# Performance work log

Hardware: AMD Instinct MI355X
Metric: run time of the kernel (lower is better)

## Reference

```python
import jax, jax.numpy as jnp
import numpy as np

LN_EPS = 1e-5

def _layernorm(x, g, b):
    mu = jnp.mean(x, axis=-1, keepdims=True)
    var = jnp.mean(jnp.square(x - mu), axis=-1, keepdims=True)
    return (x - mu) * jax.lax.rsqrt(var + LN_EPS) * g + b

def setup_inputs() -> dict:
    key = jax.random.key(0)
    ks = jax.random.split(key, 12)
    B, S, E = 8, 4096, 512
    H, DK = 64, 8          # d_k = E // H = 8 qubits per head
    NQ_FFN, FFN = 8, 2048
    TWO_PI = 2.0 * np.pi
    x = jax.random.normal(ks[0], (B, S, E), dtype=jnp.float32)
    # trainable RX phases per attention head/wire; trainable RY phases for FFN qubits
    theta_attn = jax.random.uniform(ks[1], (H, DK), dtype=jnp.float32, maxval=TWO_PI)
    theta_ffn = jax.random.uniform(ks[2], (NQ_FFN,), dtype=jnp.float32, maxval=TWO_PI)
    s_e = 1.0 / np.sqrt(E)
    W_comb = jax.random.uniform(ks[3], (E, E), dtype=jnp.float32, minval=-s_e, maxval=s_e)
    b_comb = jax.random.uniform(ks[4], (E,), dtype=jnp.float32, minval=-s_e, maxval=s_e)
    s_q = 1.0 / np.sqrt(NQ_FFN)
    W1 = jax.random.uniform(ks[5], (FFN, NQ_FFN), dtype=jnp.float32, minval=-s_q, maxval=s_q)
    b1 = jax.random.uniform(ks[6], (FFN,), dtype=jnp.float32, minval=-s_q, maxval=s_q)
    s_f = 1.0 / np.sqrt(FFN)
    W2 = jax.random.uniform(ks[7], (E, FFN), dtype=jnp.float32, minval=-s_f, maxval=s_f)
    b2 = jax.random.uniform(ks[8], (E,), dtype=jnp.float32, minval=-s_f, maxval=s_f)
    ln1_g = jnp.ones((E,), jnp.float32); ln1_b = jnp.zeros((E,), jnp.float32)
    ln2_g = jnp.ones((E,), jnp.float32); ln2_b = jnp.zeros((E,), jnp.float32)
    return {"x": x, "theta_attn": theta_attn, "W_comb": W_comb, "b_comb": b_comb,
            "ln1_g": ln1_g, "ln1_b": ln1_b, "theta_ffn": theta_ffn,
            "W1": W1, "b1": b1, "W2": W2, "b2": b2, "ln2_g": ln2_g, "ln2_b": ln2_b}

def reference(x, theta_attn, W_comb, b_comb, ln1_g, ln1_b, theta_ffn, W1, b1, W2, b2, ln2_g, ln2_b):
    B, S, E = x.shape
    H, DK = theta_attn.shape
    NQ = theta_ffn.shape[0]
    # Quantum attention heads: RX(x) then RX(theta) on |0> per wire -> <Z> = cos(x+theta)
    q = jnp.cos(x.reshape(B, S, H, DK) + theta_attn)  # [B,S,H,DK]
    attn_out = jnp.einsum('bse,fe->bsf', q.reshape(B, S, E), W_comb) + b_comb
    x1 = _layernorm(x + attn_out, ln1_g, ln1_b)
    # Quantum FFN layer: RY(x) then RY(theta) -> <Z> = cos(x+theta), first NQ features only
    fq = jnp.cos(x1[..., :NQ] + theta_ffn)            # [B,S,NQ]
    h = jax.nn.relu(jnp.einsum('bsq,fq->bsf', fq, W1) + b1)
    ffn_out = jnp.einsum('bsf,ef->bse', h, W2) + b2
    return _layernorm(x1 + ffn_out, ln2_g, ln2_b)
```

## Files before the change

kernel.cpp:

```cpp
#include <hip/hip_runtime.h>
#include <stdint.h>

typedef unsigned short u16;
typedef __bf16 bf16x8 __attribute__((ext_vector_type(8)));
typedef float f32x4 __attribute__((ext_vector_type(4)));

#define AS1(p) ((const __attribute__((address_space(1))) void*)(p))
#define AS3(p) ((__attribute__((address_space(3))) void*)(p))

__device__ __forceinline__ float b2f(u16 v){
    union { unsigned u; float f; } x; x.u = ((unsigned)v) << 16; return x.f;
}
__device__ __forceinline__ u16 f2b(float f){
    union { float f; unsigned u; } x; x.f = f;
    unsigned r = x.u + 0x7FFFu + ((x.u >> 16) & 1u);
    return (u16)(r >> 16);
}

__global__ __launch_bounds__(256) void probe_kernel(
    const u16* p0,const u16* p1,const u16* p2,const u16* p3,const u16* p4,
    const u16* p5,const u16* p6,const u16* p7,const u16* p8,const u16* p9,
    const u16* p10,const u16* p11,const u16* p12,
    int n0,int n1,int n2,int n3,int n4,int n5,int n6,int n7,int n8,int n9,
    int n10,int n11,int n12, int* flags)
{
    const u16* p; int n;
    switch (blockIdx.x) {
        case 0: p=p0; n=n0; break;   case 1: p=p1; n=n1; break;
        case 2: p=p2; n=n2; break;   case 3: p=p3; n=n3; break;
        case 4: p=p4; n=n4; break;   case 5: p=p5; n=n5; break;
        case 6: p=p6; n=n6; break;   case 7: p=p7; n=n7; break;
        case 8: p=p8; n=n8; break;   case 9: p=p9; n=n9; break;
        case 10: p=p10; n=n10; break; case 11: p=p11; n=n11; break;
        default: p=p12; n=n12; break;
    }
    int pairs = n >> 1; if (pairs > 2048) pairs = 2048;
    int strong = 0, znz = 0, tot = 0;
    for (int k = threadIdx.x; k < pairs; k += 256) {
        u16 lo = p[2*k], hi = p[2*k+1];
        int eh = (hi >> 7) & 0xFF;
        int el = (lo >> 7) & 0xFF;
        if (eh >= 0xF0 || (eh >= 1 && eh <= 0x40)) strong = 1;
        if (el >= 0xF0 || (el >= 1 && el <= 0x40)) strong = 1;
        if (lo == 0 && hi != 0) znz++;
        tot++;
    }
    __shared__ int ss, sz, st;
    if (threadIdx.x == 0) { ss = 0; sz = 0; st = 0; }
    __syncthreads();
    if (strong) atomicOr(&ss, 1);
    if (znz) atomicAdd(&sz, znz);
    atomicAdd(&st, tot);
    __syncthreads();
    if (threadIdx.x == 0) {
        flags[blockIdx.x] = (ss || (2 * sz > st)) ? 1 : 0;
        if (blockIdx.x == 0) flags[15] = 0;
    }
}

__global__ __launch_bounds__(256) void convert_kernel(
    const void* sWc, const void* sW2, const void* sW1,
    const void* sTa, const void* sBc, const void* sG1, const void* sB1l,
    const void* sTf, const void* sB1, const void* sB2, const void* sG2, const void* sB2l,
    u16* wbase, const int* flags)
{
    int b = blockIdx.x;
    const void* src; u16* dst; int n, fi, lb, tof32 = 0;
    if (b < 128)      { src=sWc; dst=wbase;          n=262144;  fi=2;  lb=b; }
    else if (b < 640) { src=sW2; dst=wbase+262144;   n=1048576; fi=9;  lb=b-128; }
    else if (b >= 643 && b < 651) { src=sW1; dst=wbase+1312256; n=16384; fi=7; lb=b-643; }
    else {
        lb = 0;
        switch (b) {
            case 640: src=sTa;  dst=wbase+1310720; n=512;  fi=1;  break;
            case 641: src=sBc;  dst=wbase+1311232; n=512;  fi=3;  break;
            case 642: src=sB2;  dst=wbase+1311744; n=512;  fi=10; break;
            case 651: src=sB1;  dst=wbase+1328640; n=2048; fi=8;  break;
            case 652: src=sG1;  dst=wbase+1330688; n=512;  fi=4;  break;
            case 653: src=sB1l; dst=wbase+1331200; n=512;  fi=5;  break;
            case 654: src=sG2;  dst=wbase+1331712; n=512;  fi=11; break;
            case 655: src=sB2l; dst=wbase+1332224; n=512;  fi=12; break;
            default:  src=sTf;  dst=wbase+1332736; n=8;    fi=6;  tof32=1; break;
        }
    }
    int i = lb * 256 + threadIdx.x;
    if (i * 8 >= n) return;
    if (tof32) {
        float* fd = (float*)dst;
        if (flags[fi]) {
            const float4* s = (const float4*)src;
            ((float4*)fd)[i*2] = s[i*2]; ((float4*)fd)[i*2+1] = s[i*2+1];
        } else {
            union { uint4 v; u16 h[8]; } sb;
            sb.v = ((const uint4*)src)[i];
            #pragma unroll
            for (int j = 0; j < 8; j++) fd[i*8+j] = b2f(sb.h[j]);
        }
        return;
    }
    if (flags[fi]) {
        const float4* s = (const float4*)src;
        float4 a = s[i*2], c = s[i*2+1];
        union { uint4 v; u16 h[8]; } o;
        o.h[0]=f2b(a.x); o.h[1]=f2b(a.y); o.h[2]=f2b(a.z); o.h[3]=f2b(a.w);
        o.h[4]=f2b(c.x); o.h[5]=f2b(c.y); o.h[6]=f2b(c.z); o.h[7]=f2b(c.w);
        ((uint4*)dst)[i] = o.v;
    } else {
        ((uint4*)dst)[i] = ((const uint4*)src)[i];
    }
}

__global__ __launch_bounds__(256) void gemm1_fused(
    const void* __restrict__ x, const u16* __restrict__ theta,
    const u16* __restrict__ Wt, const u16* __restrict__ bias,
    u16* __restrict__ dst, int mtiles, const int* flags)
{
    __shared__ __align__(16) u16 As[128 * 64];
    __shared__ __align__(16) u16 Bs[2][128 * 64];
    __shared__ __align__(16) u16 thlds[512];
    const int K = 512, N = 512;
    const int tid  = threadIdx.x;
    const int lane = tid & 63;
    const int w    = tid >> 6;

    const int blk = blockIdx.x;
    const int xcd = blk & 7;
    const int j   = blk >> 3;
    const int per = mtiles >> 3;
    const int mt  = xcd * per + (j >> 2);
    const int nt  = j & 3;
    const int m0 = mt * 128;
    const int n0 = nt * 128;

    const int srow = lane >> 3;
    const int scol = ((lane & 7) ^ srow) * 8;
    const int wm = (w >> 1) * 64;
    const int wn = (w & 1) * 64;
    const int fr   = lane & 15;
    const int quad = lane >> 4;
    const int fx   = fr & 7;

    const int genrow = tid & 127;
    const int khalf  = tid >> 7;
    const int isf32  = flags[0];

    if (tid < 64) ((uint4*)thlds)[tid] = ((const uint4*)theta)[tid];

    f32x4 acc[4][4];
    #pragma unroll
    for (int i = 0; i < 4; i++)
        #pragma unroll
        for (int jj = 0; jj < 4; jj++)
            acc[i][jj] = f32x4{0.f, 0.f, 0.f, 0.f};

    const u16* Bbase = Wt + (size_t)n0 * K + scol;

    #pragma unroll
    for (int i = 0; i < 4; i++) {
        int c = w * 4 + i;
        int row = c * 8 + srow;
        __builtin_amdgcn_global_load_lds(AS1(Bbase + (size_t)row * K),
                                         AS3(&Bs[0][c * 512]), 16, 0, 0);
    }
    uint4 xr[8];
    {
        size_t eoff = (size_t)(m0 + genrow) * 512 + khalf * 32;
        if (isf32) {
            const uint4* p = (const uint4*)x + (eoff >> 2);
            #pragma unroll
            for (int i = 0; i < 8; i++) xr[i] = p[i];
        } else {
            const uint4* p = (const uint4*)x + (eoff >> 3);
            #pragma unroll
            for (int i = 0; i < 4; i++) xr[i] = p[i];
        }
    }

    int cur = 0;
    for (int kt = 0; kt < K; kt += 64) {
        __syncthreads();
        {
            float xv[32];
            if (isf32) {
                const float* xf = (const float*)xr;
                #pragma unroll
                for (int i2 = 0; i2 < 32; i2++) xv[i2] = xf[i2];
            } else {
                const u16* xh = (const u16*)xr;
                #pragma unroll
                for (int i2 = 0; i2 < 32; i2++) xv[i2] = b2f(xh[i2]);
            }
            int tbase = (kt + khalf * 32) >> 3;
            #pragma unroll
            for (int jj = 0; jj < 4; jj++) {
                union { uint4 v; u16 h[8]; } tb;
                tb.v = ((const uint4*)thlds)[tbase + jj];
                union { uint4 v; __bf16 h[8]; } ob;
                #pragma unroll
                for (int e = 0; e < 8; e++)
                    ob.h[e] = (__bf16)__cosf(xv[jj * 8 + e] + b2f(tb.h[e]));
                int o = khalf * 4 + jj;
                *(uint4*)(As + genrow * 64 + ((o ^ (genrow & 7)) * 8)) = ob.v;
            }
        }
        __syncthreads();
        if (kt + 64 < K) {
            size_t eoff = (size_t)(m0 + genrow) * 512 + kt + 64 + khalf * 32;
            if (isf32) {
                const uint4* p = (const uint4*)x + (eoff >> 2);
                #pragma unroll
                for (int i = 0; i < 8; i++) xr[i] = p[i];
            } else {
                const uint4* p = (const uint4*)x + (eoff >> 3);
                #pragma unroll
                for (int i = 0; i < 4; i++) xr[i] = p[i];
            }
            int nxt = cur ^ 1;
            #pragma unroll
            for (int i = 0; i < 4; i++) {
                int c = w * 4 + i;
                int row = c * 8 + srow;
                __builtin_amdgcn_global_load_lds(
                    AS1(Bbase + (size_t)row * K + kt + 64),
                    AS3(&Bs[nxt][c * 512]), 16, 0, 0);
            }
        }
        #pragma unroll
        for (int kk = 0; kk < 2; kk++) {
            bf16x8 af[4], bfr[4];
            #pragma unroll
            for (int mi = 0; mi < 4; mi++)
                af[mi] = *(const bf16x8*)(As + (wm + mi * 16 + fr) * 64 +
                                          (((kk * 4 + quad) ^ fx) * 8));
            #pragma unroll
            for (int ni = 0; ni < 4; ni++)
                bfr[ni] = *(const bf16x8*)(&Bs[cur][(wn + ni * 16 + fr) * 64 +
                                           (((kk * 4 + quad) ^ fx) * 8)]);
            #pragma unroll
            for (int mi = 0; mi < 4; mi++)
                #pragma unroll
                for (int ni = 0; ni < 4; ni++)
                    acc[mi][ni] = __builtin_amdgcn_mfma_f32_16x16x32_bf16(
                        af[mi], bfr[ni], acc[mi][ni], 0, 0, 0);
        }
        cur ^= 1;
    }

    #pragma unroll
    for (int mi = 0; mi < 4; mi++) {
        #pragma unroll
        for (int ni = 0; ni < 4; ni++) {
            int n = n0 + wn + ni * 16 + fr;
            float bn = b2f(bias[n]);
            #pragma unroll
            for (int r = 0; r < 4; r++) {
                int m = m0 + wm + mi * 16 + quad * 4 + r;
                float rv = isf32 ? ((const float*)x)[(size_t)m * N + n]
                                 : b2f(((const u16*)x)[(size_t)m * N + n]);
                dst[(size_t)m * N + n] = f2b(acc[mi][ni][r] + bn + rv);
            }
        }
    }
}

__global__ __launch_bounds__(256) void gemm2_fused(
    const u16* __restrict__ fq, const u16* __restrict__ W1, const u16* __restrict__ b1,
    const u16* __restrict__ Wt, const u16* __restrict__ bias,
    const u16* __restrict__ res, u16* __restrict__ dst, int mtiles)
{
    __shared__ __align__(16) u16 As[128 * 64];
    __shared__ __align__(16) u16 Bs[2][128 * 64];
    const int K = 2048, N = 512;
    const int tid  = threadIdx.x;
    const int lane = tid & 63;
    const int w    = tid >> 6;

    const int blk = blockIdx.x;
    const int xcd = blk & 7;
    const int j   = blk >> 3;
    const int per = mtiles >> 3;
    const int mt  = xcd * per + (j >> 2);
    const int nt  = j & 3;
    const int m0 = mt * 128;
    const int n0 = nt * 128;

    const int srow = lane >> 3;
    const int scol = ((lane & 7) ^ srow) * 8;
    const int wm = (w >> 1) * 64;
    const int wn = (w & 1) * 64;
    const int fr   = lane & 15;
    const int quad = lane >> 4;
    const int fx   = fr & 7;

    bf16x8 fqf[8];
    #pragma unroll
    for (int t2 = 0; t2 < 8; t2++) {
        union { uint4 v; bf16x8 b; } z; z.v = uint4{0,0,0,0};
        if (quad == 0) z.v = *(const uint4*)(fq + (size_t)(m0 + t2 * 16 + fr) * 8);
        fqf[t2] = z.b;
    }
    union { uint4 v; bf16x8 b; } w1u; w1u.v = uint4{0,0,0,0};
    if (quad == 0) w1u.v = *(const uint4*)(W1 + (size_t)(w * 16 + fr) * 8);
    uint2 b1v = *(const uint2*)(b1 + w * 16 + quad * 4);

    f32x4 acc[4][4];
    #pragma unroll
    for (int i = 0; i < 4; i++)
        #pragma unroll
        for (int jj = 0; jj < 4; jj++)
            acc[i][jj] = f32x4{0.f, 0.f, 0.f, 0.f};

    const u16* Bbase = Wt + (size_t)n0 * K + scol;
    #pragma unroll
    for (int i = 0; i < 4; i++) {
        int c = w * 4 + i;
        int row = c * 8 + srow;
        __builtin_amdgcn_global_load_lds(AS1(Bbase + (size_t)row * K),
                                         AS3(&Bs[0][c * 512]), 16, 0, 0);
    }

    int cur = 0;
    for (int kt = 0; kt < K; kt += 64) {
        __syncthreads();
        {
            const u16* pb = (const u16*)&b1v;
            f32x4 binit = {b2f(pb[0]), b2f(pb[1]), b2f(pb[2]), b2f(pb[3])};
            const int g   = w * 2 + (quad >> 1);
            const int off = (quad & 1) * 4;
            #pragma unroll
            for (int t2 = 0; t2 < 8; t2++) {
                f32x4 hv = __builtin_amdgcn_mfma_f32_16x16x32_bf16(
                    w1u.b, fqf[t2], binit, 0, 0, 0);
                union { uint2 u; __bf16 h[4]; } hw;
                hw.h[0] = (__bf16)fmaxf(hv[0], 0.f);
                hw.h[1] = (__bf16)fmaxf(hv[1], 0.f);
                hw.h[2] = (__bf16)fmaxf(hv[2], 0.f);
                hw.h[3] = (__bf16)fmaxf(hv[3], 0.f);
                int m = t2 * 16 + fr;
                *(uint2*)(As + m * 64 + ((g ^ (m & 7)) * 8 + off)) = hw.u;
            }
        }
        __syncthreads();
        if (kt + 64 < K) {
            if (quad == 0)
                w1u.v = *(const uint4*)(W1 + (size_t)(kt + 64 + w * 16 + fr) * 8);
            b1v = *(const uint2*)(b1 + kt + 64 + w * 16 + quad * 4);
            int nxt = cur ^ 1;
            #pragma unroll
            for (int i = 0; i < 4; i++) {
                int c = w * 4 + i;
                int row = c * 8 + srow;
                __builtin_amdgcn_global_load_lds(
                    AS1(Bbase + (size_t)row * K + kt + 64),
                    AS3(&Bs[nxt][c * 512]), 16, 0, 0);
            }
        }
        #pragma unroll
        for (int kk = 0; kk < 2; kk++) {
            bf16x8 af[4], bfr[4];
            #pragma unroll
            for (int mi = 0; mi < 4; mi++)
                af[mi] = *(const bf16x8*)(As + (wm + mi * 16 + fr) * 64 +
                                          (((kk * 4 + quad) ^ fx) * 8));
            #pragma unroll
            for (int ni = 0; ni < 4; ni++)
                bfr[ni] = *(const bf16x8*)(&Bs[cur][(wn + ni * 16 + fr) * 64 +
                                           (((kk * 4 + quad) ^ fx) * 8)]);
            #pragma unroll
            for (int mi = 0; mi < 4; mi++)
                #pragma unroll
                for (int ni = 0; ni < 4; ni++)
                    acc[mi][ni] = __builtin_amdgcn_mfma_f32_16x16x32_bf16(
                        af[mi], bfr[ni], acc[mi][ni], 0, 0, 0);
        }
        cur ^= 1;
    }

    #pragma unroll
    for (int mi = 0; mi < 4; mi++) {
        #pragma unroll
        for (int ni = 0; ni < 4; ni++) {
            int n = n0 + wn + ni * 16 + fr;
            float bn = b2f(bias[n]);
            #pragma unroll
            for (int r = 0; r < 4; r++) {
                int m = m0 + wm + mi * 16 + quad * 4 + r;
                float rv = b2f(res[(size_t)m * N + n]);
                dst[(size_t)m * N + n] = f2b(acc[mi][ni][r] + bn + rv);
            }
        }
    }
}

__global__ __launch_bounds__(512) void ln1_kernel(
    const u16* __restrict__ y1, const u16* __restrict__ g, const u16* __restrict__ b,
    const float* __restrict__ tf, u16* __restrict__ x1, u16* __restrict__ fqout)
{
    __shared__ __align__(16) float xs8[64][8];
    const int t = threadIdx.x;
    const int wv = t >> 6, l = t & 63;
    const size_t rbase = (size_t)blockIdx.x * 64;

    union { uint4 v; u16 s[8]; } gb, bb;
    gb.v = *(const uint4*)(g + l * 8);
    bb.v = *(const uint4*)(b + l * 8);

    #pragma unroll
    for (int i = 0; i < 8; i++) {
        int lr = wv * 8 + i;
        union { uint4 v; u16 s[8]; } yb;
        yb.v = ((const uint4*)(y1 + (rbase + lr) * 512))[l];
        float xv[8], s = 0.f, ss = 0.f;
        #pragma unroll
        for (int jj = 0; jj < 8; jj++) {
            xv[jj] = b2f(yb.s[jj]); s += xv[jj]; ss += xv[jj] * xv[jj];
        }
        #pragma unroll
        for (int o = 32; o > 0; o >>= 1) { s += __shfl_down(s, o); ss += __shfl_down(ss, o); }
        s = __shfl(s, 0); ss = __shfl(ss, 0);
        float mu = s * (1.f / 512.f);
        float rs = rsqrtf(ss * (1.f / 512.f) - mu * mu + 1e-5f);
        union { uint4 v; u16 s[8]; } ob;
        float xn[8];
        #pragma unroll
        for (int jj = 0; jj < 8; jj++) {
            xn[jj] = (xv[jj] - mu) * rs * b2f(gb.s[jj]) + b2f(bb.s[jj]);
            ob.s[jj] = f2b(xn[jj]);
        }
        ((uint4*)(x1 + (rbase + lr) * 512))[l] = ob.v;
        if (l == 0) {
            #pragma unroll
            for (int jj = 0; jj < 8; jj++) xs8[lr][jj] = xn[jj];
        }
    }
    __syncthreads();
    {
        int r = t >> 3, jj = t & 7;
        fqout[(rbase + r) * 8 + jj] = f2b(__cosf(xs8[r][jj] + tf[jj]));
    }
}

__global__ __launch_bounds__(256) void ln2_kernel(
    const u16* __restrict__ z, const u16* __restrict__ g, const u16* __restrict__ b,
    void* __restrict__ out, const int* flags)
{
    const int t = threadIdx.x;
    const int wv = t >> 6, l = t & 63;
    const size_t row = (size_t)blockIdx.x * 4 + wv;

    union { uint4 v; u16 s[8]; } zb, gb, bb;
    zb.v = ((const uint4*)(z + row * 512))[l];
    gb.v = *(const uint4*)(g + l * 8);
    bb.v = *(const uint4*)(b + l * 8);
    float xv[8], s = 0.f, ss = 0.f;
    #pragma unroll
    for (int jj = 0; jj < 8; jj++) { xv[jj] = b2f(zb.s[jj]); s += xv[jj]; ss += xv[jj]*xv[jj]; }
    #pragma unroll
    for (int o = 32; o > 0; o >>= 1) { s += __shfl_down(s, o); ss += __shfl_down(ss, o); }
    s = __shfl(s, 0); ss = __shfl(ss, 0);
    float mu = s * (1.f / 512.f);
    float rs = rsqrtf(ss * (1.f / 512.f) - mu * mu + 1e-5f);
    float xn[8];
    #pragma unroll
    for (int jj = 0; jj < 8; jj++)
        xn[jj] = (xv[jj] - mu) * rs * b2f(gb.s[jj]) + b2f(bb.s[jj]);
    if (flags[0]) {
        float* po = (float*)out + row * 512 + l * 8;
        float4 o0{xn[0],xn[1],xn[2],xn[3]}, o1{xn[4],xn[5],xn[6],xn[7]};
        *(float4*)po = o0; *(float4*)(po + 4) = o1;
    } else {
        union { uint4 v; u16 s[8]; } ob;
        #pragma unroll
        for (int jj = 0; jj < 8; jj++) ob.s[jj] = f2b(xn[jj]);
        ((uint4*)((u16*)out + row * 512))[l] = ob.v;
    }
}

extern "C" void kernel_launch(void* const* d_in, const int* in_sizes, int n_in,
                              void* d_out, int out_size, void* d_ws, size_t ws_size,
                              hipStream_t stream)
{
    u16* ws16 = (u16*)d_ws;
    u16* W     = ws16;
    int* flags = (int*)(ws16 + 1332752);
    u16* fq  = ws16 + 1332800;
    u16* x1  = ws16 + 1594944;
    u16* y1  = ws16 + 18372160;
    u16* z   = y1;

    const u16*  wWc  = W;
    const u16*  wW2  = W + 262144;
    const u16*  wTa  = W + 1310720;
    const u16*  wBc  = W + 1311232;
    const u16*  wB2  = W + 1311744;
    const u16*  wW1  = W + 1312256;
    const u16*  wB1  = W + 1328640;
    const u16*  wG1  = W + 1330688;
    const u16*  wB1l = W + 1331200;
    const u16*  wG2  = W + 1331712;
    const u16*  wB2l = W + 1332224;
    const float* wTf = (const float*)(W + 1332736);

    probe_kernel<<<13, 256, 0, stream>>>(
        (const u16*)d_in[0], (const u16*)d_in[1], (const u16*)d_in[2],
        (const u16*)d_in[3], (const u16*)d_in[4], (const u16*)d_in[5],
        (const u16*)d_in[6], (const u16*)d_in[7], (const u16*)d_in[8],
        (const u16*)d_in[9], (const u16*)d_in[10], (const u16*)d_in[11],
        (const u16*)d_in[12],
        in_sizes[0], in_sizes[1], in_sizes[2], in_sizes[3], in_sizes[4],
        in_sizes[5], in_sizes[6], in_sizes[7], in_sizes[8], in_sizes[9],
        in_sizes[10], in_sizes[11], in_sizes[12], flags);

    convert_kernel<<<657, 256, 0, stream>>>(
        d_in[2], d_in[9], d_in[7], d_in[1], d_in[3], d_in[4], d_in[5],
        d_in[6], d_in[8], d_in[10], d_in[11], d_in[12], (u16*)W, flags);

    gemm1_fused<<<1024, 256, 0, stream>>>(
        d_in[0], wTa, wWc, wBc, y1, 256, flags);

    ln1_kernel<<<512, 512, 0, stream>>>(y1, wG1, wB1l, wTf, x1, fq);

    gemm2_fused<<<1024, 256, 0, stream>>>(
        fq, wW1, wB1, wW2, wB2, x1, z, 256);

    ln2_kernel<<<8192, 256, 0, stream>>>(z, wG2, wB2l, d_out, flags);
}
```

Baseline: 352.2 us.

## Compute cos(x+theta) A-fragments directly from global memory in gemm1

Removes the shared-memory staging tile for the A operand in the first GEMM. Each wave now loads x straight from global memory into its MFMA fragment registers and applies cos(x+theta) there. This drops one LDS buffer and one barrier per k-step and adds a launch-bounds occupancy hint. The cost is that x loads are no longer prefetched a step ahead, so load latency sits in the MFMA loop. The cosine is also recomputed by both waves that share the same rows (wn split), doubling the transcendental work and x reads.

```diff
diff --git a/kernel.cpp b/kernel.cpp
--- a/kernel.cpp
+++ b/kernel.cpp
@@ -110,12 +110,11 @@
     }
 }
 
-__global__ __launch_bounds__(256) void gemm1_fused(
+__global__ __launch_bounds__(256, 4) void gemm1_fused(
     const void* __restrict__ x, const u16* __restrict__ theta,
     const u16* __restrict__ Wt, const u16* __restrict__ bias,
     u16* __restrict__ dst, int mtiles, const int* flags)
 {
-    __shared__ __align__(16) u16 As[128 * 64];
     __shared__ __align__(16) u16 Bs[2][128 * 64];
     __shared__ __align__(16) u16 thlds[512];
     const int K = 512, N = 512;
@@ -139,10 +138,7 @@
     const int fr   = lane & 15;
     const int quad = lane >> 4;
     const int fx   = fr & 7;
-
-    const int genrow = tid & 127;
-    const int khalf  = tid >> 7;
-    const int isf32  = flags[0];
+    const int isf32 = flags[0];
 
     if (tid < 64) ((uint4*)thlds)[tid] = ((const uint4*)theta)[tid];
 
@@ -162,59 +158,11 @@
         __builtin_amdgcn_global_load_lds(AS1(Bbase + (size_t)row * K),
                                          AS3(&Bs[0][c * 512]), 16, 0, 0);
     }
-    uint4 xr[8];
-    {
-        size_t eoff = (size_t)(m0 + genrow) * 512 + khalf * 32;
-        if (isf32) {
-            const uint4* p = (const uint4*)x + (eoff >> 2);
-            #pragma unroll
-            for (int i = 0; i < 8; i++) xr[i] = p[i];
-        } else {
-            const uint4* p = (const uint4*)x + (eoff >> 3);
-            #pragma unroll
-            for (int i = 0; i < 4; i++) xr[i] = p[i];
-        }
-    }
 
     int cur = 0;
     for (int kt = 0; kt < K; kt += 64) {
         __syncthreads();
-        {
-            float xv[32];
-            if (isf32) {
-                const float* xf = (const float*)xr;
-                #pragma unroll
-                for (int i2 = 0; i2 < 32; i2++) xv[i2] = xf[i2];
-            } else {
-                const u16* xh = (const u16*)xr;
-                #pragma unroll
-                for (int i2 = 0; i2 < 32; i2++) xv[i2] = b2f(xh[i2]);
-            }
-            int tbase = (kt + khalf * 32) >> 3;
-            #pragma unroll
-            for (int jj = 0; jj < 4; jj++) {
-                union { uint4 v; u16 h[8]; } tb;
-                tb.v = ((const uint4*)thlds)[tbase + jj];
-                union { uint4 v; __bf16 h[8]; } ob;
-                #pragma unroll
-                for (int e = 0; e < 8; e++)
-                    ob.h[e] = (__bf16)__cosf(xv[jj * 8 + e] + b2f(tb.h[e]));
-                int o = khalf * 4 + jj;
-                *(uint4*)(As + genrow * 64 + ((o ^ (genrow & 7)) * 8)) = ob.v;
-            }
-        }
-        __syncthreads();
         if (kt + 64 < K) {
-            size_t eoff = (size_t)(m0 + genrow) * 512 + kt + 64 + khalf * 32;
-            if (isf32) {
-                const uint4* p = (const uint4*)x + (eoff >> 2);
-                #pragma unroll
-                for (int i = 0; i < 8; i++) xr[i] = p[i];
-            } else {
-                const uint4* p = (const uint4*)x + (eoff >> 3);
-                #pragma unroll
-                for (int i = 0; i < 4; i++) xr[i] = p[i];
-            }
             int nxt = cur ^ 1;
             #pragma unroll
             for (int i = 0; i < 4; i++) {
@@ -227,11 +175,33 @@
         }
         #pragma unroll
         for (int kk = 0; kk < 2; kk++) {
-            bf16x8 af[4], bfr[4];
-            #pragma unroll
-            for (int mi = 0; mi < 4; mi++)
-                af[mi] = *(const bf16x8*)(As + (wm + mi * 16 + fr) * 64 +
-                                          (((kk * 4 + quad) ^ fx) * 8));
+            const int kb = kt + kk * 32 + quad * 8;
+            union { uint4 v; u16 h[8]; } tb;
+            tb.v = *(const uint4*)(thlds + kb);
+            float th[8];
+            #pragma unroll
+            for (int e = 0; e < 8; e++) th[e] = b2f(tb.h[e]);
+            bf16x8 af[4];
+            #pragma unroll
+            for (int mi = 0; mi < 4; mi++) {
+                size_t ro = (size_t)(m0 + wm + mi * 16 + fr) * 512 + kb;
+                float xv[8];
+                if (isf32) {
+                    const float4* xp = (const float4*)((const float*)x + ro);
+                    float4 a = xp[0], b = xp[1];
+                    xv[0]=a.x; xv[1]=a.y; xv[2]=a.z; xv[3]=a.w;
+                    xv[4]=b.x; xv[5]=b.y; xv[6]=b.z; xv[7]=b.w;
+                } else {
+                    union { uint4 v; u16 h[8]; } xb;
+                    xb.v = *(const uint4*)((const u16*)x + ro);
+                    #pragma unroll
+                    for (int e = 0; e < 8; e++) xv[e] = b2f(xb.h[e]);
+                }
+                #pragma unroll
+                for (int e = 0; e < 8; e++)
+                    af[mi][e] = (__bf16)__cosf(xv[e] + th[e]);
+            }
+            bf16x8 bfr[4];
             #pragma unroll
             for (int ni = 0; ni < 4; ni++)
                 bfr[ni] = *(const bf16x8*)(&Bs[cur][(wn + ni * 16 + fr) * 64 +
```

Result: slower. 581.8 us (+65.2%).
